# Kernel tuning notes

Measured on AMD Instinct MI355X. Metric: run time of the kernel, lower is better.

## Reference

```python
import jax, jax.numpy as jnp
import numpy as np
from jax import lax

ITERS = 10
EPS = 1e-6
LOSS_WEIGHT = 1.0


def _max_pool3x3(x):
    # F.max_pool2d(x, kernel_size=3, stride=1, padding=1): torch pads with -inf for max pool
    return lax.reduce_window(x, -jnp.inf, lax.max,
                             window_dimensions=(1, 1, 3, 3),
                             window_strides=(1, 1, 1, 1),
                             padding=((0, 0), (0, 0), (1, 1), (1, 1)))


def _soft_erode(x):
    return -_max_pool3x3(-x)


def _soft_dilate(x):
    return _max_pool3x3(x)


def _soft_open(x):
    return _soft_dilate(_soft_erode(x))


def _soft_skel(img, iters):
    img = jnp.clip(img, 0.0, 1.0)
    img1 = _soft_open(img)
    skel = jax.nn.relu(img - img1)
    for _ in range(iters):
        img = _soft_erode(img)
        img1 = _soft_open(img)
        delta = jax.nn.relu(img - img1)
        skel = skel + jax.nn.relu(delta - skel * delta)
    return skel


def setup_inputs() -> dict:
    key = jax.random.key(0)
    k1, k2 = jax.random.split(key)
    B, C, H, W = 8, 2, 1024, 1024
    pred = jax.random.normal(k1, (B, C, H, W), dtype=jnp.float32)
    target = jax.random.uniform(k2, (B, C, H, W), dtype=jnp.float32)
    return {"pred": pred, "target": target}


def reference(pred, target):
    # sigmoid on logits
    p = jax.nn.sigmoid(pred)  # [B,C,H,W]
    t = target.astype(p.dtype)
    # per-class channel slicing is equivalent to channel-wise ops (pooling is per-channel)
    skel_p = _soft_skel(p, ITERS)
    skel_t = _soft_skel(t, ITERS)
    hw = (2, 3)
    tprec = jnp.sum(skel_p * t, axis=hw) / (jnp.sum(skel_p, axis=hw) + EPS)  # [B,C]
    tsens = jnp.sum(skel_t * p, axis=hw) / (jnp.sum(skel_t, axis=hw) + EPS)  # [B,C]
    cl_dice = 1.0 - 2.0 * tprec * tsens / (tprec + tsens + EPS)  # [B,C]
    # original: per-class mean over batch, then mean over classes == global mean
    return LOSS_WEIGHT * jnp.mean(cl_dice)
```

## Files before the change

### kernel.cpp

```cpp
#include <hip/hip_runtime.h>


#define IMG 1024
#define NBC 16
#define LEPS 1e-6f

typedef unsigned int u32;

__device__ __forceinline__ u32 pk_min(u32 a, u32 b) {
    u32 d; asm("v_pk_min_f16 %0, %1, %2" : "=v"(d) : "v"(a), "v"(b)); return d;
}
__device__ __forceinline__ u32 pk_max(u32 a, u32 b) {
    u32 d; asm("v_pk_max_f16 %0, %1, %2" : "=v"(d) : "v"(a), "v"(b)); return d;
}
__device__ __forceinline__ u32 pk_max0(u32 a) {
    u32 d; asm("v_pk_max_f16 %0, %1, 0" : "=v"(d) : "v"(a)); return d;
}
__device__ __forceinline__ u32 pk_add(u32 a, u32 b) {
    u32 d; asm("v_pk_add_f16 %0, %1, %2" : "=v"(d) : "v"(a), "v"(b)); return d;
}
__device__ __forceinline__ u32 pk_fma(u32 a, u32 b, u32 c) {
    u32 d; asm("v_pk_fma_f16 %0, %1, %2, %3" : "=v"(d) : "v"(a), "v"(b), "v"(c)); return d;
}
__device__ __forceinline__ u32 dpp_prev(u32 x) {
    return (u32)__builtin_amdgcn_update_dpp(0, (int)x, 0x130, 0xf, 0xf, true);
}
__device__ __forceinline__ u32 dpp_next(u32 x) {
    return (u32)__builtin_amdgcn_update_dpp(0, (int)x, 0x138, 0xf, 0xf, true);
}
__device__ __forceinline__ u32 alignh(u32 hi, u32 lo) {
    return __builtin_amdgcn_alignbit(hi, lo, 16);
}
__device__ __forceinline__ u32 swap16(u32 x) { return alignh(x, x); }
__device__ __forceinline__ float sigmoidf(float x) { return 1.0f / (1.0f + __expf(-x)); }

#define STEP(SRC, DST)                                                          \
    {                                                                           \
        u32 pv = SRC[0];                                                        \
        _Pragma("unroll")                                                       \
        for (int r = 1; r <= 38; ++r) {                                         \
            u32 v = pk_min(pk_min(pv, SRC[r]), SRC[r + 1]);                     \
            pv = SRC[r];                                                        \
            u32 dm = dpp_prev(v);                                               \
            u32 dp = dpp_next(v);                                               \
            DST[r] = pk_min(pk_min(alignh(v, dm), v), alignh(dp, v));           \
        }                                                                       \
        _Pragma("unroll")                                                       \
        for (int r = 12; r <= 27; ++r) {                                        \
            u32 up = (r == 12) ? (edgeT ? DST[12] : DST[11]) : DST[r - 1];      \
            u32 dn = (r == 27) ? (edgeB ? DST[27] : DST[28]) : DST[r + 1];      \
            u32 v = pk_max(pk_max(up, DST[r]), dn);                             \
            u32 dm = dpp_prev(v);                                               \
            u32 dp = dpp_next(v);                                               \
            u32 m = pk_max(pk_max(alignh(v, dm), v), alignh(dp, v));            \
            if (edgeL) {              \
                u32 pm = pk_max(v, swap16(v));                                  \
                if (lane == 6) m = (m & 0xFFFF0000u) | (pm & 0xFFFFu);          \
            }                                                                   \
            if (edgeR) {    \
                u32 pm = pk_max(v, swap16(v));                                  \
                if (lane == 49) m = (m & 0x0000FFFFu) | (pm & 0xFFFF0000u);     \
            }                                                                   \
            u32 d = pk_max0(pk_add(SRC[r], m ^ 0x80008000u));                   \
            u32 t = pk_max0(pk_fma(nS[r - 12], d, d));                          \
            nS[r - 12] = pk_add(nS[r - 12], t ^ 0x80008000u);                   \
        }                                                                       \
    }

__global__ __launch_bounds__(256, 3)
void skel_wave_kernel(const float* __restrict__ pred,
                      const float* __restrict__ target,
                      float* __restrict__ ws)
{
    const int tid    = threadIdx.x;
    const int lane   = tid & 63;
    const int waveId = tid >> 6;

    const int bc  = blockIdx.z & (NBC - 1);
    const int img = blockIdx.z >> 4;
    const int tr0 = (blockIdx.y * 4 + waveId) * 16;
    const int cb0 = blockIdx.x * 104;
    const int wc0 = cb0 - 12;

    const float* src = (img == 0) ? pred : target;
    const size_t base = (size_t)bc * (size_t)(IMG * IMG);

    const bool edgeT = (tr0 == 0);
    const bool edgeB = (tr0 == IMG - 16);
    const bool edgeL = (blockIdx.x == 0);
    const bool edgeR = (blockIdx.x == 9);

    const int ic0 = wc0 + 2 * lane;

    u32 A[40], B[40];
#pragma unroll
    for (int i = 0; i < 40; ++i) {
        int ir = min(max(tr0 - 12 + i, 0), IMG - 1);
        const float* rowp = src + base + (size_t)ir * IMG;
        float a, b;
        if (!(edgeL || edgeR)) {
            float2 f2 = *(const float2*)(rowp + ic0);
            a = f2.x; b = f2.y;
        } else {
            a = rowp[min(max(ic0, 0), IMG - 1)];
            b = rowp[min(max(ic0 + 1, 0), IMG - 1)];
        }
        if (img == 0) { a = sigmoidf(a); b = sigmoidf(b); }
        else { a = fminf(fmaxf(a, 0.f), 1.f); b = fminf(fmaxf(b, 0.f), 1.f); }
        _Float16 ha = (_Float16)a, hb = (_Float16)b;
        unsigned short ua, ub;
        __builtin_memcpy(&ua, &ha, 2);
        __builtin_memcpy(&ub, &hb, 2);
        A[i] = (u32)ua | ((u32)ub << 16);
    }
    B[0] = A[0];
    B[39] = A[39];

    u32 nS[16];
#pragma unroll
    for (int j = 0; j < 16; ++j) nS[j] = 0u;

    STEP(A, B)
#pragma unroll 1
    for (int p = 0; p < 5; ++p) {
        STEP(B, A)
        STEP(A, B)
    }

    const int wlo = 2 * lane, whi = 2 * lane + 1;
    const float mLo = (wlo >= 12 && wlo <= 115 && ic0 <= IMG - 1) ? 1.f : 0.f;
    const float mHi = (whi >= 12 && whi <= 115 && ic0 + 1 <= IMG - 1) ? 1.f : 0.f;

    const float* osrc = (img == 0) ? target : pred;
    float s_sum = 0.f, sp_sum = 0.f;
#pragma unroll
    for (int j = 0; j < 16; ++j) {
        int ir = tr0 + j;
        const float* rowp = osrc + base + (size_t)ir * IMG;
        float oa, ob;
        if (!(edgeL || edgeR)) {
            float2 f2 = *(const float2*)(rowp + ic0);
            oa = f2.x; ob = f2.y;
        } else {
            oa = rowp[min(max(ic0, 0), IMG - 1)];
            ob = rowp[min(max(ic0 + 1, 0), IMG - 1)];
        }
        if (img == 1) { oa = sigmoidf(oa); ob = sigmoidf(ob); }
        unsigned short ul = (unsigned short)(nS[j] & 0xFFFFu);
        unsigned short uh = (unsigned short)(nS[j] >> 16);
        _Float16 hl, hh;
        __builtin_memcpy(&hl, &ul, 2);
        __builtin_memcpy(&hh, &uh, 2);
        float svLo = -(float)hl * mLo;
        float svHi = -(float)hh * mHi;
        s_sum  += svLo + svHi;
        sp_sum += svLo * oa + svHi * ob;
    }

#pragma unroll
    for (int off = 32; off > 0; off >>= 1) {
        s_sum  += __shfl_down(s_sum,  off, 64);
        sp_sum += __shfl_down(sp_sum, off, 64);
    }
    if (lane == 0) {
        float* acc = ws + (size_t)blockIdx.z * 2;
        atomicAdd(acc + 0, sp_sum);
        atomicAdd(acc + 1, s_sum);
    }
}

__global__ void finalize_kernel(const float* __restrict__ ws, float* __restrict__ out)
{
    if (threadIdx.x == 0) {
        float acc = 0.0f;
        for (int bc = 0; bc < NBC; ++bc) {
            float spt = ws[(0 * NBC + bc) * 2 + 0];
            float sp  = ws[(0 * NBC + bc) * 2 + 1];
            float stp = ws[(1 * NBC + bc) * 2 + 0];
            float st  = ws[(1 * NBC + bc) * 2 + 1];
            float tprec = spt / (sp + LEPS);
            float tsens = stp / (st + LEPS);
            acc += 1.0f - 2.0f * tprec * tsens / (tprec + tsens + LEPS);
        }
        out[0] = acc / (float)NBC;
    }
}

extern "C" void kernel_launch(void* const* d_in, const int* in_sizes, int n_in,
                              void* d_out, int out_size, void* d_ws, size_t ws_size,
                              hipStream_t stream) {
    const float* pred   = (const float*)d_in[0];
    const float* target = (const float*)d_in[1];
    float* ws  = (float*)d_ws;
    float* out = (float*)d_out;

    hipMemsetAsync(d_ws, 0, 2 * NBC * 2 * sizeof(float), stream);

    dim3 grid(10, 16, 2 * NBC);
    skel_wave_kernel<<<grid, 256, 0, stream>>>(pred, target, ws);
    finalize_kernel<<<1, 64, 0, stream>>>(ws, out);
}
```

Baseline: 594.3 us.

## Erode in place with a single register buffer and raise occupancy to four waves

The ping-pong A/B register buffers are replaced by one 40-row buffer P that is updated in place. Each row's horizontal min is computed first and then combined vertically, and a 16-row copy E keeps the pre-erosion center rows for the skeleton update. The dilation is also done horizontal-first, and the iteration loop becomes a single loop of 11 steps. The register saving is used to request four waves per EU instead of three, to hide latency better, at the cost of a few extra horizontal ops and some duplicated edge-lane logic.

```diff
diff --git a/kernel.cpp b/kernel.cpp
--- a/kernel.cpp
+++ b/kernel.cpp
@@ -34,40 +34,17 @@
 __device__ __forceinline__ u32 swap16(u32 x) { return alignh(x, x); }
 __device__ __forceinline__ float sigmoidf(float x) { return 1.0f / (1.0f + __expf(-x)); }
 
-#define STEP(SRC, DST)                                                          \
-    {                                                                           \
-        u32 pv = SRC[0];                                                        \
-        _Pragma("unroll")                                                       \
-        for (int r = 1; r <= 38; ++r) {                                         \
-            u32 v = pk_min(pk_min(pv, SRC[r]), SRC[r + 1]);                     \
-            pv = SRC[r];                                                        \
-            u32 dm = dpp_prev(v);                                               \
-            u32 dp = dpp_next(v);                                               \
-            DST[r] = pk_min(pk_min(alignh(v, dm), v), alignh(dp, v));           \
-        }                                                                       \
-        _Pragma("unroll")                                                       \
-        for (int r = 12; r <= 27; ++r) {                                        \
-            u32 up = (r == 12) ? (edgeT ? DST[12] : DST[11]) : DST[r - 1];      \
-            u32 dn = (r == 27) ? (edgeB ? DST[27] : DST[28]) : DST[r + 1];      \
-            u32 v = pk_max(pk_max(up, DST[r]), dn);                             \
-            u32 dm = dpp_prev(v);                                               \
-            u32 dp = dpp_next(v);                                               \
-            u32 m = pk_max(pk_max(alignh(v, dm), v), alignh(dp, v));            \
-            if (edgeL) {              \
-                u32 pm = pk_max(v, swap16(v));                                  \
-                if (lane == 6) m = (m & 0xFFFF0000u) | (pm & 0xFFFFu);          \
-            }                                                                   \
-            if (edgeR) {    \
-                u32 pm = pk_max(v, swap16(v));                                  \
-                if (lane == 49) m = (m & 0x0000FFFFu) | (pm & 0xFFFF0000u);     \
-            }                                                                   \
-            u32 d = pk_max0(pk_add(SRC[r], m ^ 0x80008000u));                   \
-            u32 t = pk_max0(pk_fma(nS[r - 12], d, d));                          \
-            nS[r - 12] = pk_add(nS[r - 12], t ^ 0x80008000u);                   \
-        }                                                                       \
-    }
-
-__global__ __launch_bounds__(256, 3)
+__device__ __forceinline__ u32 hmin3(u32 x) {
+    u32 dm = dpp_prev(x), dp = dpp_next(x);
+    return pk_min(pk_min(alignh(x, dm), x), alignh(dp, x));
+}
+__device__ __forceinline__ u32 hmax3(u32 x) {
+    u32 dm = dpp_prev(x), dp = dpp_next(x);
+    return pk_max(pk_max(alignh(x, dm), x), alignh(dp, x));
+}
+
+__global__ __launch_bounds__(256)
+__attribute__((amdgpu_waves_per_eu(4, 4)))
 void skel_wave_kernel(const float* __restrict__ pred,
                       const float* __restrict__ target,
                       float* __restrict__ ws)
@@ -92,7 +69,7 @@
 
     const int ic0 = wc0 + 2 * lane;
 
-    u32 A[40], B[40];
+    u32 P[40];
 #pragma unroll
     for (int i = 0; i < 40; ++i) {
         int ir = min(max(tr0 - 12 + i, 0), IMG - 1);
@@ -111,20 +88,57 @@
         unsigned short ua, ub;
         __builtin_memcpy(&ua, &ha, 2);
         __builtin_memcpy(&ub, &hb, 2);
-        A[i] = (u32)ua | ((u32)ub << 16);
-    }
-    B[0] = A[0];
-    B[39] = A[39];
-
+        P[i] = (u32)ua | ((u32)ub << 16);
+    }
+
+    u32 E[16];
     u32 nS[16];
 #pragma unroll
     for (int j = 0; j < 16; ++j) nS[j] = 0u;
 
-    STEP(A, B)
 #pragma unroll 1
-    for (int p = 0; p < 5; ++p) {
-        STEP(B, A)
-        STEP(A, B)
+    for (int k = 0; k < 11; ++k) {
+        {
+            u32 hm1 = hmin3(P[0]);
+            u32 h0  = hmin3(P[1]);
+#pragma unroll
+            for (int r = 1; r <= 38; ++r) {
+                u32 hp1 = hmin3(P[r + 1]);
+                if (r >= 12 && r <= 27) E[r - 12] = P[r];
+                P[r] = pk_min(pk_min(hm1, h0), hp1);
+                hm1 = h0; h0 = hp1;
+            }
+        }
+
+        {
+            u32 gm1 = hmax3(edgeT ? P[12] : P[11]);
+            u32 g0  = hmax3(P[12]);
+#pragma unroll
+            for (int j = 12; j <= 27; ++j) {
+                u32 gp1 = hmax3((j == 27) ? (edgeB ? P[27] : P[28]) : P[j + 1]);
+                u32 m = pk_max(pk_max(gm1, g0), gp1);
+                gm1 = g0; g0 = gp1;
+
+                if (edgeL) {
+                    u32 up = (j == 12 && edgeT) ? P[12] : P[j - 1];
+                    u32 dn = (j == 27 && edgeB) ? P[27] : P[j + 1];
+                    u32 v  = pk_max(pk_max(up, P[j]), dn);
+                    u32 pm = pk_max(v, swap16(v));
+                    if (lane == 6) m = (m & 0xFFFF0000u) | (pm & 0xFFFFu);
+                }
+                if (edgeR) {
+                    u32 up = (j == 12 && edgeT) ? P[12] : P[j - 1];
+                    u32 dn = (j == 27 && edgeB) ? P[27] : P[j + 1];
+                    u32 v  = pk_max(pk_max(up, P[j]), dn);
+                    u32 pm = pk_max(v, swap16(v));
+                    if (lane == 49) m = (m & 0x0000FFFFu) | (pm & 0xFFFF0000u);
+                }
+
+                u32 d = pk_max0(pk_add(E[j - 12], m ^ 0x80008000u));
+                u32 t = pk_max0(pk_fma(nS[j - 12], d, d));
+                nS[j - 12] = pk_add(nS[j - 12], t ^ 0x80008000u);
+            }
+        }
     }
 
     const int wlo = 2 * lane, whi = 2 * lane + 1;
```

Result: no change. 600.1 us (+1.0%).
